# Kernel optimization log

Hardware: AMD Instinct MI355X
Metric: run time of the kernel (lower is better)

Reference implementation:

```python
import jax, jax.numpy as jnp
import numpy as np

B, T, V, E, H = 32, 40, 8000, 50, 2048


def setup_inputs() -> dict:
    key = jax.random.key(0)
    ks = jax.random.split(key, 13)
    s = 0.02  # small init scale for stability
    return {
        "features": jax.random.normal(ks[0], (B, H), dtype=jnp.float32),
        "captions": jax.random.randint(ks[1], (B, T), 0, V),
        "emb": jax.random.normal(ks[2], (V, E), dtype=jnp.float32) * s,
        "lstm_Wih": jax.random.normal(ks[3], (4 * H, E), dtype=jnp.float32) * s,
        "lstm_bih": jax.random.normal(ks[4], (4 * H,), dtype=jnp.float32) * s,
        "lstm_Whh": jax.random.normal(ks[5], (4 * H, H), dtype=jnp.float32) * s,
        "lstm_bhh": jax.random.normal(ks[6], (4 * H,), dtype=jnp.float32) * s,
        "gru_Wih": jax.random.normal(ks[7], (3 * H, H), dtype=jnp.float32) * s,
        "gru_bih": jax.random.normal(ks[8], (3 * H,), dtype=jnp.float32) * s,
        "gru_Whh": jax.random.normal(ks[9], (3 * H, H), dtype=jnp.float32) * s,
        "gru_bhh": jax.random.normal(ks[10], (3 * H,), dtype=jnp.float32) * s,
        "lin_W": jax.random.normal(ks[11], (V, H), dtype=jnp.float32) * s,
        "lin_b": jax.random.normal(ks[12], (V,), dtype=jnp.float32) * s,
    }


def reference(features, captions, emb, lstm_Wih, lstm_bih, lstm_Whh, lstm_bhh,
              gru_Wih, gru_bih, gru_Whh, gru_bhh, lin_W, lin_b):
    # Dropout layers act as identity in eval mode.
    embeddings = emb[captions]                 # [B, T, E]
    xs = jnp.swapaxes(embeddings[:, :-1], 0, 1)  # [T-1, B, E]

    def step(carry, x):
        h_l, c_l, h_g = carry
        # torch LSTMCell
        gates = x @ lstm_Wih.T + lstm_bih + h_l @ lstm_Whh.T + lstm_bhh
        i, f, g, o = jnp.split(gates, 4, axis=-1)
        c = jax.nn.sigmoid(f) * c_l + jax.nn.sigmoid(i) * jnp.tanh(g)
        h = jax.nn.sigmoid(o) * jnp.tanh(c)
        # torch GRUCell, input = lstm cell state c
        gi = c @ gru_Wih.T + gru_bih
        gh = h_g @ gru_Whh.T + gru_bhh
        r_i, z_i, n_i = jnp.split(gi, 3, axis=-1)
        r_h, z_h, n_h = jnp.split(gh, 3, axis=-1)
        r = jax.nn.sigmoid(r_i + r_h)
        z = jax.nn.sigmoid(z_i + z_h)
        n = jnp.tanh(n_i + r * n_h)
        hg = (1.0 - z) * n + z * h_g
        out = hg @ lin_W.T + lin_b              # [B, V]
        return (h, c, hg), out

    init = (features, features, features)
    _, outs = jax.lax.scan(step, init, xs)      # [T-1, B, V]
    return jnp.swapaxes(outs, 0, 1)             # [B, T-1, V]
```

## Files before the change

kernel.cpp:

```cpp
#include <hip/hip_runtime.h>

#define BB 32
#define TT 40
#define TS 39
#define VV 8000
#define EE 50
#define HH 2048

typedef short s16x8 __attribute__((ext_vector_type(8)));
typedef float f32x4 __attribute__((ext_vector_type(4)));

__device__ __forceinline__ float sigmf(float x) { return 1.0f / (1.0f + __expf(-x)); }
__device__ __forceinline__ float tanhf_fast(float x) { return 2.0f / (1.0f + __expf(-2.0f * x)) - 1.0f; }

__device__ __forceinline__ unsigned short f2bf(float x) {
    union { float f; unsigned u; } v; v.f = x;
    unsigned r = v.u + 0x7FFF + ((v.u >> 16) & 1);
    return (unsigned short)(r >> 16);
}

__global__ void convert_kernel(const float* __restrict__ src,
                               unsigned short* __restrict__ dst, int n4) {
    int i = blockIdx.x * 256 + threadIdx.x;
    if (i < n4) {
        float4 v = ((const float4*)src)[i];
        ushort4 o;
        o.x = f2bf(v.x); o.y = f2bf(v.y); o.z = f2bf(v.z); o.w = f2bf(v.w);
        ((ushort4*)dst)[i] = o;
    }
}

__global__ void embed_proj_kernel(const int* __restrict__ caps,
                                  const float* __restrict__ emb,
                                  const float* __restrict__ Wih,
                                  const float* __restrict__ bih,
                                  const float* __restrict__ bhh,
                                  float* __restrict__ xw) {
    __shared__ float elds[BB][EE];
    int t = blockIdx.y;
    int j = blockIdx.x * 256 + threadIdx.x;
    for (int idx = threadIdx.x; idx < BB * EE; idx += 256) {
        int bl = idx / EE, e = idx - bl * EE;
        elds[bl][e] = emb[(size_t)caps[bl * TT + t] * EE + e];
    }
    __syncthreads();
    float wreg[EE];
#pragma unroll
    for (int e = 0; e < EE; ++e) wreg[e] = Wih[(size_t)j * EE + e];
    float bias = bih[j] + bhh[j];
    for (int bl = 0; bl < BB; ++bl) {
        float acc = bias;
#pragma unroll
        for (int e = 0; e < EE; ++e) acc += wreg[e] * elds[bl][e];
        xw[((size_t)(t * BB + bl)) * (4 * HH) + j] = acc;
    }
}

__global__ void init_state_kernel(const float* __restrict__ feat,
                                  float* __restrict__ c32, float* __restrict__ hg32,
                                  unsigned short* __restrict__ hbf,
                                  unsigned short* __restrict__ cbf,
                                  unsigned short* __restrict__ hgbf) {
    int i = blockIdx.x * 256 + threadIdx.x;
    float v = feat[i];
    c32[i] = v; hg32[i] = v;
    unsigned short b = f2bf(v);
    hbf[i] = b; cbf[i] = b; hgbf[i] = b;
}

__global__ __launch_bounds__(1024, 4) void step1_kernel(
    const unsigned short* __restrict__ Whh,
    const unsigned short* __restrict__ gWhh,
    const float* __restrict__ gbhh,
    const float* __restrict__ xw_t,
    const unsigned short* __restrict__ hbf_in,
    const unsigned short* __restrict__ hgbf,
    float* __restrict__ c32,
    unsigned short* __restrict__ cbf,
    unsigned short* __restrict__ hbf_out,
    float* __restrict__ gh)
{
    __shared__ float lsum[4][4][32][17];
    const int tid = threadIdx.x;
    const int lane = tid & 63;
    const int w = tid >> 6;
    const int g = w >> 2;
    const int kh = w & 3;
    const int l15 = lane & 15;
    const int lq = lane >> 4;
    const int kofs = kh * 512 + lq * 8;

    const bool lstm = (blockIdx.x < 128);
    const unsigned short* Abase;
    const unsigned short* Brow;
    if (lstm) {
        int kk0 = blockIdx.x * 16;
        Brow = Whh + (size_t)(g * HH + kk0 + l15) * HH + kofs;
        Abase = hbf_in;
    } else {
        int n0 = (blockIdx.x - 128) * 64;
        Brow = gWhh + (size_t)(n0 + g * 16 + l15) * HH + kofs;
        Abase = hgbf;
    }
    const unsigned short* Arow0 = Abase + l15 * HH + kofs;
    const unsigned short* Arow1 = Arow0 + 16 * HH;

    f32x4 acc0 = {0.f, 0.f, 0.f, 0.f};
    f32x4 acc1 = {0.f, 0.f, 0.f, 0.f};
#pragma unroll 4
    for (int it = 0; it < 16; ++it) {
        s16x8 bv = *(const s16x8*)(Brow + it * 32);
        s16x8 a0 = *(const s16x8*)(Arow0 + it * 32);
        s16x8 a1 = *(const s16x8*)(Arow1 + it * 32);
        acc0 = __builtin_amdgcn_mfma_f32_16x16x32_bf16(a0, bv, acc0, 0, 0, 0);
        acc1 = __builtin_amdgcn_mfma_f32_16x16x32_bf16(a1, bv, acc1, 0, 0, 0);
    }
#pragma unroll
    for (int r = 0; r < 4; ++r) {
        lsum[g][kh][lq * 4 + r][l15]      = acc0[r];
        lsum[g][kh][16 + lq * 4 + r][l15] = acc1[r];
    }
    __syncthreads();

    if (lstm) {
        if (tid < 512) {
            int kk0 = blockIdx.x * 16;
            int kkl = tid & 15, b = tid >> 4;
            int kk = kk0 + kkl;
            const float* xwb = xw_t + (size_t)b * 4 * HH;
            float vi = lsum[0][0][b][kkl] + lsum[0][1][b][kkl] + lsum[0][2][b][kkl] + lsum[0][3][b][kkl] + xwb[kk];
            float vf = lsum[1][0][b][kkl] + lsum[1][1][b][kkl] + lsum[1][2][b][kkl] + lsum[1][3][b][kkl] + xwb[HH + kk];
            float vg = lsum[2][0][b][kkl] + lsum[2][1][b][kkl] + lsum[2][2][b][kkl] + lsum[2][3][b][kkl] + xwb[2 * HH + kk];
            float vo = lsum[3][0][b][kkl] + lsum[3][1][b][kkl] + lsum[3][2][b][kkl] + lsum[3][3][b][kkl] + xwb[3 * HH + kk];
            int idx = b * HH + kk;
            float c = sigmf(vf) * c32[idx] + sigmf(vi) * tanhf_fast(vg);
            float h = sigmf(vo) * tanhf_fast(c);
            c32[idx] = c;
            cbf[idx] = f2bf(c);
            hbf_out[idx] = f2bf(h);
        }
    } else {
        int n0 = (blockIdx.x - 128) * 64;
        for (int cell = tid; cell < 2048; cell += 1024) {
            int nl = cell & 63, b = cell >> 6;
            int s = nl >> 4, n15 = nl & 15;
            float v = lsum[s][0][b][n15] + lsum[s][1][b][n15] + lsum[s][2][b][n15] + lsum[s][3][b][n15]
                      + gbhh[n0 + nl];
            gh[b * 3 * HH + n0 + nl] = v;
        }
    }
}

__global__ __launch_bounds__(768, 3) void step2_kernel(
    const unsigned short* __restrict__ gWih,
    const float* __restrict__ gbih,
    const unsigned short* __restrict__ cbf,
    const float* __restrict__ gh,
    float* __restrict__ hg32,
    unsigned short* __restrict__ hgbf,
    unsigned short* __restrict__ hg_all_t)
{
    __shared__ float lsum[3][4][32][17];
    const int tid = threadIdx.x;
    const int lane = tid & 63;
    const int w = tid >> 6;
    const int g = w >> 2;
    const int kh = w & 3;
    const int l15 = lane & 15;
    const int lq = lane >> 4;
    const int kofs = kh * 512 + lq * 8;
    const int kk0 = blockIdx.x * 16;

    const unsigned short* Arow0 = cbf + l15 * HH + kofs;
    const unsigned short* Arow1 = Arow0 + 16 * HH;
    const unsigned short* Brow = gWih + (size_t)(g * HH + kk0 + l15) * HH + kofs;

    f32x4 acc0 = {0.f, 0.f, 0.f, 0.f};
    f32x4 acc1 = {0.f, 0.f, 0.f, 0.f};
#pragma unroll 4
    for (int it = 0; it < 16; ++it) {
        s16x8 bv = *(const s16x8*)(Brow + it * 32);
        s16x8 a0 = *(const s16x8*)(Arow0 + it * 32);
        s16x8 a1 = *(const s16x8*)(Arow1 + it * 32);
        acc0 = __builtin_amdgcn_mfma_f32_16x16x32_bf16(a0, bv, acc0, 0, 0, 0);
        acc1 = __builtin_amdgcn_mfma_f32_16x16x32_bf16(a1, bv, acc1, 0, 0, 0);
    }
#pragma unroll
    for (int r = 0; r < 4; ++r) {
        lsum[g][kh][lq * 4 + r][l15]      = acc0[r];
        lsum[g][kh][16 + lq * 4 + r][l15] = acc1[r];
    }
    __syncthreads();

    if (tid < 512) {
        int kkl = tid & 15, b = tid >> 4;
        int kk = kk0 + kkl;
        float ri = lsum[0][0][b][kkl] + lsum[0][1][b][kkl] + lsum[0][2][b][kkl] + lsum[0][3][b][kkl] + gbih[kk];
        float zi = lsum[1][0][b][kkl] + lsum[1][1][b][kkl] + lsum[1][2][b][kkl] + lsum[1][3][b][kkl] + gbih[HH + kk];
        float ni = lsum[2][0][b][kkl] + lsum[2][1][b][kkl] + lsum[2][2][b][kkl] + lsum[2][3][b][kkl] + gbih[2 * HH + kk];
        const float* ghb = gh + b * 3 * HH;
        float r = sigmf(ri + ghb[kk]);
        float z = sigmf(zi + ghb[HH + kk]);
        float n = tanhf_fast(ni + r * ghb[2 * HH + kk]);
        int idx = b * HH + kk;
        float hgn = (1.f - z) * n + z * hg32[idx];
        hg32[idx] = hgn;
        unsigned short hb = f2bf(hgn);
        hgbf[idx] = hb;
        hg_all_t[idx] = hb;
    }
}

__global__ __launch_bounds__(256) void out_gemm_kernel(
    const unsigned short* __restrict__ A,
    const unsigned short* __restrict__ Wl,
    const float* __restrict__ bl,
    float* __restrict__ out) {
    __shared__ unsigned short As[128][32];
    __shared__ unsigned short Bs[128][32];
    const int tid = threadIdx.x;
    const int lane = tid & 63;
    const int w = tid >> 6;
    const int l15 = lane & 15;
    const int lq = lane >> 4;
    const int mt = blockIdx.x, nt = blockIdx.y;
    const int mq = w >> 1, nq = w & 1;

    const int row0 = tid >> 2, kc0 = (tid & 3) * 8;
    const unsigned short* Ap0 = A + (size_t)(mt * 128 + row0) * HH + kc0;
    const unsigned short* Ap1 = A + (size_t)(mt * 128 + 64 + row0) * HH + kc0;
    const unsigned short* Bp0 = Wl + (size_t)(nt * 128 + row0) * HH + kc0;
    const unsigned short* Bp1 = Wl + (size_t)(nt * 128 + 64 + row0) * HH + kc0;

    f32x4 acc[4][4];
#pragma unroll
    for (int i = 0; i < 4; ++i)
#pragma unroll
        for (int j = 0; j < 4; ++j) acc[i][j] = (f32x4){0.f, 0.f, 0.f, 0.f};

    for (int k0 = 0; k0 < HH; k0 += 32) {
        s16x8 a0v = *(const s16x8*)(Ap0 + k0);
        s16x8 a1v = *(const s16x8*)(Ap1 + k0);
        s16x8 b0v = *(const s16x8*)(Bp0 + k0);
        s16x8 b1v = *(const s16x8*)(Bp1 + k0);
        *(s16x8*)&As[row0][kc0]      = a0v;
        *(s16x8*)&As[64 + row0][kc0] = a1v;
        *(s16x8*)&Bs[row0][kc0]      = b0v;
        *(s16x8*)&Bs[64 + row0][kc0] = b1v;
        __syncthreads();
        s16x8 af[4], bf[4];
#pragma unroll
        for (int i = 0; i < 4; ++i) af[i] = *(const s16x8*)&As[mq * 64 + i * 16 + l15][lq * 8];
#pragma unroll
        for (int j = 0; j < 4; ++j) bf[j] = *(const s16x8*)&Bs[nq * 64 + j * 16 + l15][lq * 8];
#pragma unroll
        for (int i = 0; i < 4; ++i)
#pragma unroll
            for (int j = 0; j < 4; ++j)
                acc[i][j] = __builtin_amdgcn_mfma_f32_16x16x32_bf16(af[i], bf[j], acc[i][j], 0, 0, 0);
        __syncthreads();
    }
#pragma unroll
    for (int j = 0; j < 4; ++j) {
        int n = nt * 128 + nq * 64 + j * 16 + l15;
        float bn = bl[n < VV ? n : VV - 1];
#pragma unroll
        for (int i = 0; i < 4; ++i) {
#pragma unroll
            for (int r = 0; r < 4; ++r) {
                int m = mt * 128 + mq * 64 + i * 16 + lq * 4 + r;
                if (m < TS * BB && n < VV) {
                    int t = m >> 5, b = m & 31;
                    out[((size_t)b * TS + t) * VV + n] = acc[i][j][r] + bn;
                }
            }
        }
    }
}

extern "C" void kernel_launch(void* const* d_in, const int* in_sizes, int n_in,
                              void* d_out, int out_size, void* d_ws, size_t ws_size,
                              hipStream_t stream) {
    const float* features = (const float*)d_in[0];
    const int*   captions = (const int*)d_in[1];
    const float* emb      = (const float*)d_in[2];
    const float* lstm_Wih = (const float*)d_in[3];
    const float* lstm_bih = (const float*)d_in[4];
    const float* lstm_Whh = (const float*)d_in[5];
    const float* lstm_bhh = (const float*)d_in[6];
    const float* gru_Wih  = (const float*)d_in[7];
    const float* gru_bih  = (const float*)d_in[8];
    const float* gru_Whh  = (const float*)d_in[9];
    const float* gru_bhh  = (const float*)d_in[10];
    const float* lin_W    = (const float*)d_in[11];
    const float* lin_b    = (const float*)d_in[12];
    float* out = (float*)d_out;

    unsigned short* us = (unsigned short*)d_ws;
    unsigned short* Whh_bf  = us;
    unsigned short* gWhh_bf = Whh_bf  + (size_t)8192 * HH;
    unsigned short* gWih_bf = gWhh_bf + (size_t)6144 * HH;
    unsigned short* linW_bf = gWih_bf + (size_t)6144 * HH;
    unsigned short* hbf0    = linW_bf + (size_t)VV * HH;
    unsigned short* hbf1    = hbf0 + BB * HH;
    unsigned short* cbf     = hbf1 + BB * HH;
    unsigned short* hgbf    = cbf  + BB * HH;
    unsigned short* hg_all  = hgbf + BB * HH;
    float* f32s = (float*)(hg_all + (size_t)1280 * HH);
    float* xw   = f32s;
    float* c32  = xw + (size_t)TS * BB * 4 * HH;
    float* hg32 = c32 + BB * HH;
    float* gh   = hg32 + BB * HH;

    {
        int n4;
        n4 = 8192 * HH / 4;
        convert_kernel<<<(n4 + 255) / 256, 256, 0, stream>>>(lstm_Whh, Whh_bf, n4);
        n4 = 6144 * HH / 4;
        convert_kernel<<<(n4 + 255) / 256, 256, 0, stream>>>(gru_Whh, gWhh_bf, n4);
        convert_kernel<<<(n4 + 255) / 256, 256, 0, stream>>>(gru_Wih, gWih_bf, n4);
        n4 = VV * HH / 4;
        convert_kernel<<<(n4 + 255) / 256, 256, 0, stream>>>(lin_W, linW_bf, n4);
    }

    embed_proj_kernel<<<dim3(4 * HH / 256, TS), 256, 0, stream>>>(
        captions, emb, lstm_Wih, lstm_bih, lstm_bhh, xw);

    init_state_kernel<<<(BB * HH) / 256, 256, 0, stream>>>(
        features, c32, hg32, hbf0, cbf, hgbf);

    for (int t = 0; t < TS; ++t) {
        const unsigned short* hin = (t & 1) ? hbf1 : hbf0;
        unsigned short*       hout = (t & 1) ? hbf0 : hbf1;
        step1_kernel<<<224, 1024, 0, stream>>>(
            Whh_bf, gWhh_bf, gru_bhh, xw + (size_t)t * BB * 4 * HH,
            hin, hgbf, c32, cbf, hout, gh);
        step2_kernel<<<128, 768, 0, stream>>>(
            gWih_bf, gru_bih, cbf, gh, hg32, hgbf, hg_all + (size_t)t * BB * HH);
    }

    out_gemm_kernel<<<dim3((TS * BB + 127) / 128, (VV + 127) / 128), 256, 0, stream>>>(
        hg_all, linW_bf, lin_b, out);
}
```

Measured before the change: 2.054 ms.

## Fuse per-timestep recurrent kernels into one persistent cooperative kernel with grid sync

Replaces the 78 per-step launches of step1/step2 with a single cooperative kernel of 256 blocks that loops over all timesteps and uses grid.sync between the LSTM/GRU-hidden phase and the GRU-input phase. It targets launch overhead and inter-kernel gaps on a latency-bound recurrence. In exchange, grid-wide barriers replace kernel boundaries, some blocks sit idle in each phase, and the kernel relies on all 256 blocks of 1024 threads being co-resident.

```diff
diff --git a/kernel.cpp b/kernel.cpp
--- a/kernel.cpp
+++ b/kernel.cpp
@@ -1,4 +1,7 @@
 #include <hip/hip_runtime.h>
+#include <hip/hip_cooperative_groups.h>
+
+namespace cg = cooperative_groups;
 
 #define BB 32
 #define TT 40
@@ -68,146 +71,144 @@
     hbf[i] = b; cbf[i] = b; hgbf[i] = b;
 }
 
-__global__ __launch_bounds__(1024, 4) void step1_kernel(
-    const unsigned short* __restrict__ Whh,
-    const unsigned short* __restrict__ gWhh,
-    const float* __restrict__ gbhh,
-    const float* __restrict__ xw_t,
-    const unsigned short* __restrict__ hbf_in,
-    const unsigned short* __restrict__ hgbf,
-    float* __restrict__ c32,
-    unsigned short* __restrict__ cbf,
-    unsigned short* __restrict__ hbf_out,
-    float* __restrict__ gh)
-{
+struct PKArgs {
+    const unsigned short* Whh;
+    const unsigned short* gWhh;
+    const unsigned short* gWih;
+    const float* gbhh;
+    const float* gbih;
+    const float* xw;
+    float* c32;
+    float* hg32;
+    float* gh;
+    unsigned short* hbf0;
+    unsigned short* hbf1;
+    unsigned short* cbf;
+    unsigned short* hgbf;
+    unsigned short* hg_all;
+};
+
+__global__ __launch_bounds__(1024, 4) void persistent_step_kernel(PKArgs p) {
+    cg::grid_group grid = cg::this_grid();
     __shared__ float lsum[4][4][32][17];
     const int tid = threadIdx.x;
     const int lane = tid & 63;
     const int w = tid >> 6;
+    const int l15 = lane & 15;
+    const int lq = lane >> 4;
+    const int bx = blockIdx.x;
+
     const int g = w >> 2;
     const int kh = w & 3;
-    const int l15 = lane & 15;
-    const int lq = lane >> 4;
     const int kofs = kh * 512 + lq * 8;
 
-    const bool lstm = (blockIdx.x < 128);
-    const unsigned short* Abase;
-    const unsigned short* Brow;
-    if (lstm) {
-        int kk0 = blockIdx.x * 16;
-        Brow = Whh + (size_t)(g * HH + kk0 + l15) * HH + kofs;
-        Abase = hbf_in;
-    } else {
-        int n0 = (blockIdx.x - 128) * 64;
-        Brow = gWhh + (size_t)(n0 + g * 16 + l15) * HH + kofs;
-        Abase = hgbf;
-    }
-    const unsigned short* Arow0 = Abase + l15 * HH + kofs;
-    const unsigned short* Arow1 = Arow0 + 16 * HH;
-
-    f32x4 acc0 = {0.f, 0.f, 0.f, 0.f};
-    f32x4 acc1 = {0.f, 0.f, 0.f, 0.f};
+    const unsigned short* Brow1 = nullptr;
+    if (bx < 128) {
+        Brow1 = p.Whh + (size_t)(g * HH + bx * 16 + l15) * HH + kofs;
+    } else if (bx < 224) {
+        Brow1 = p.gWhh + (size_t)((bx - 128) * 64 + g * 16 + l15) * HH + kofs;
+    }
+    const unsigned short* Brow2 = nullptr;
+    if (bx < 128 && w < 12) {
+        Brow2 = p.gWih + (size_t)(g * HH + bx * 16 + l15) * HH + kofs;
+    }
+
+    for (int t = 0; t < TS; ++t) {
+        const unsigned short* hin  = (t & 1) ? p.hbf1 : p.hbf0;
+        unsigned short*       hout = (t & 1) ? p.hbf0 : p.hbf1;
+        const float* xw_t = p.xw + (size_t)t * BB * 4 * HH;
+
+        if (bx < 224) {
+            const unsigned short* Abase = (bx < 128) ? hin : p.hgbf;
+            const unsigned short* Arow0 = Abase + l15 * HH + kofs;
+            const unsigned short* Arow1 = Arow0 + 16 * HH;
+            f32x4 acc0 = {0.f, 0.f, 0.f, 0.f};
+            f32x4 acc1 = {0.f, 0.f, 0.f, 0.f};
 #pragma unroll 4
-    for (int it = 0; it < 16; ++it) {
-        s16x8 bv = *(const s16x8*)(Brow + it * 32);
-        s16x8 a0 = *(const s16x8*)(Arow0 + it * 32);
-        s16x8 a1 = *(const s16x8*)(Arow1 + it * 32);
-        acc0 = __builtin_amdgcn_mfma_f32_16x16x32_bf16(a0, bv, acc0, 0, 0, 0);
-        acc1 = __builtin_amdgcn_mfma_f32_16x16x32_bf16(a1, bv, acc1, 0, 0, 0);
-    }
-#pragma unroll
-    for (int r = 0; r < 4; ++r) {
-        lsum[g][kh][lq * 4 + r][l15]      = acc0[r];
-        lsum[g][kh][16 + lq * 4 + r][l15] = acc1[r];
-    }
-    __syncthreads();
-
-    if (lstm) {
-        if (tid < 512) {
-            int kk0 = blockIdx.x * 16;
+            for (int it = 0; it < 16; ++it) {
+                s16x8 bv = *(const s16x8*)(Brow1 + it * 32);
+                s16x8 a0 = *(const s16x8*)(Arow0 + it * 32);
+                s16x8 a1 = *(const s16x8*)(Arow1 + it * 32);
+                acc0 = __builtin_amdgcn_mfma_f32_16x16x32_bf16(a0, bv, acc0, 0, 0, 0);
+                acc1 = __builtin_amdgcn_mfma_f32_16x16x32_bf16(a1, bv, acc1, 0, 0, 0);
+            }
+#pragma unroll
+            for (int r = 0; r < 4; ++r) {
+                lsum[g][kh][lq * 4 + r][l15]      = acc0[r];
+                lsum[g][kh][16 + lq * 4 + r][l15] = acc1[r];
+            }
+        }
+        __syncthreads();
+
+        if (bx < 128) {
+            if (tid < 512) {
+                int kk0 = bx * 16;
+                int kkl = tid & 15, b = tid >> 4;
+                int kk = kk0 + kkl;
+                const float* xwb = xw_t + (size_t)b * 4 * HH;
+                float vi = lsum[0][0][b][kkl] + lsum[0][1][b][kkl] + lsum[0][2][b][kkl] + lsum[0][3][b][kkl] + xwb[kk];
+                float vf = lsum[1][0][b][kkl] + lsum[1][1][b][kkl] + lsum[1][2][b][kkl] + lsum[1][3][b][kkl] + xwb[HH + kk];
+                float vg = lsum[2][0][b][kkl] + lsum[2][1][b][kkl] + lsum[2][2][b][kkl] + lsum[2][3][b][kkl] + xwb[2 * HH + kk];
+                float vo = lsum[3][0][b][kkl] + lsum[3][1][b][kkl] + lsum[3][2][b][kkl] + lsum[3][3][b][kkl] + xwb[3 * HH + kk];
+                int idx = b * HH + kk;
+                float c = sigmf(vf) * p.c32[idx] + sigmf(vi) * tanhf_fast(vg);
+                float h = sigmf(vo) * tanhf_fast(c);
+                p.c32[idx] = c;
+                p.cbf[idx] = f2bf(c);
+                hout[idx] = f2bf(h);
+            }
+        } else if (bx < 224) {
+            int n0 = (bx - 128) * 64;
+            for (int cell = tid; cell < 2048; cell += 1024) {
+                int nl = cell & 63, b = cell >> 6;
+                int s = nl >> 4, n15 = nl & 15;
+                float v = lsum[s][0][b][n15] + lsum[s][1][b][n15] + lsum[s][2][b][n15] + lsum[s][3][b][n15]
+                          + p.gbhh[n0 + nl];
+                p.gh[b * 3 * HH + n0 + nl] = v;
+            }
+        }
+        grid.sync();
+
+        if (bx < 128 && w < 12) {
+            const unsigned short* Arow0 = p.cbf + l15 * HH + kofs;
+            const unsigned short* Arow1 = Arow0 + 16 * HH;
+            f32x4 acc0 = {0.f, 0.f, 0.f, 0.f};
+            f32x4 acc1 = {0.f, 0.f, 0.f, 0.f};
+#pragma unroll 4
+            for (int it = 0; it < 16; ++it) {
+                s16x8 bv = *(const s16x8*)(Brow2 + it * 32);
+                s16x8 a0 = *(const s16x8*)(Arow0 + it * 32);
+                s16x8 a1 = *(const s16x8*)(Arow1 + it * 32);
+                acc0 = __builtin_amdgcn_mfma_f32_16x16x32_bf16(a0, bv, acc0, 0, 0, 0);
+                acc1 = __builtin_amdgcn_mfma_f32_16x16x32_bf16(a1, bv, acc1, 0, 0, 0);
+            }
+#pragma unroll
+            for (int r = 0; r < 4; ++r) {
+                lsum[g][kh][lq * 4 + r][l15]      = acc0[r];
+                lsum[g][kh][16 + lq * 4 + r][l15] = acc1[r];
+            }
+        }
+        __syncthreads();
+
+        if (bx < 128 && tid < 512) {
+            int kk0 = bx * 16;
             int kkl = tid & 15, b = tid >> 4;
             int kk = kk0 + kkl;
-            const float* xwb = xw_t + (size_t)b * 4 * HH;
-            float vi = lsum[0][0][b][kkl] + lsum[0][1][b][kkl] + lsum[0][2][b][kkl] + lsum[0][3][b][kkl] + xwb[kk];
-            float vf = lsum[1][0][b][kkl] + lsum[1][1][b][kkl] + lsum[1][2][b][kkl] + lsum[1][3][b][kkl] + xwb[HH + kk];
-            float vg = lsum[2][0][b][kkl] + lsum[2][1][b][kkl] + lsum[2][2][b][kkl] + lsum[2][3][b][kkl] + xwb[2 * HH + kk];
-            float vo = lsum[3][0][b][kkl] + lsum[3][1][b][kkl] + lsum[3][2][b][kkl] + lsum[3][3][b][kkl] + xwb[3 * HH + kk];
+            float ri = lsum[0][0][b][kkl] + lsum[0][1][b][kkl] + lsum[0][2][b][kkl] + lsum[0][3][b][kkl] + p.gbih[kk];
+            float zi = lsum[1][0][b][kkl] + lsum[1][1][b][kkl] + lsum[1][2][b][kkl] + lsum[1][3][b][kkl] + p.gbih[HH + kk];
+            float ni = lsum[2][0][b][kkl] + lsum[2][1][b][kkl] + lsum[2][2][b][kkl] + lsum[2][3][b][kkl] + p.gbih[2 * HH + kk];
+            const float* ghb = p.gh + b * 3 * HH;
+            float r = sigmf(ri + ghb[kk]);
+            float z = sigmf(zi + ghb[HH + kk]);
+            float n = tanhf_fast(ni + r * ghb[2 * HH + kk]);
             int idx = b * HH + kk;
-            float c = sigmf(vf) * c32[idx] + sigmf(vi) * tanhf_fast(vg);
-            float h = sigmf(vo) * tanhf_fast(c);
-            c32[idx] = c;
-            cbf[idx] = f2bf(c);
-            hbf_out[idx] = f2bf(h);
-        }
-    } else {
-        int n0 = (blockIdx.x - 128) * 64;
-        for (int cell = tid; cell < 2048; cell += 1024) {
-            int nl = cell & 63, b = cell >> 6;
-            int s = nl >> 4, n15 = nl & 15;
-            float v = lsum[s][0][b][n15] + lsum[s][1][b][n15] + lsum[s][2][b][n15] + lsum[s][3][b][n15]
-                      + gbhh[n0 + nl];
-            gh[b * 3 * HH + n0 + nl] = v;
-        }
-    }
-}
-
-__global__ __launch_bounds__(768, 3) void step2_kernel(
-    const unsigned short* __restrict__ gWih,
-    const float* __restrict__ gbih,
-    const unsigned short* __restrict__ cbf,
-    const float* __restrict__ gh,
-    float* __restrict__ hg32,
-    unsigned short* __restrict__ hgbf,
-    unsigned short* __restrict__ hg_all_t)
-{
-    __shared__ float lsum[3][4][32][17];
-    const int tid = threadIdx.x;
-    const int lane = tid & 63;
-    const int w = tid >> 6;
-    const int g = w >> 2;
-    const int kh = w & 3;
-    const int l15 = lane & 15;
-    const int lq = lane >> 4;
-    const int kofs = kh * 512 + lq * 8;
-    const int kk0 = blockIdx.x * 16;
-
-    const unsigned short* Arow0 = cbf + l15 * HH + kofs;
-    const unsigned short* Arow1 = Arow0 + 16 * HH;
-    const unsigned short* Brow = gWih + (size_t)(g * HH + kk0 + l15) * HH + kofs;
-
-    f32x4 acc0 = {0.f, 0.f, 0.f, 0.f};
-    f32x4 acc1 = {0.f, 0.f, 0.f, 0.f};
-#pragma unroll 4
-    for (int it = 0; it < 16; ++it) {
-        s16x8 bv = *(const s16x8*)(Brow + it * 32);
-        s16x8 a0 = *(const s16x8*)(Arow0 + it * 32);
-        s16x8 a1 = *(const s16x8*)(Arow1 + it * 32);
-        acc0 = __builtin_amdgcn_mfma_f32_16x16x32_bf16(a0, bv, acc0, 0, 0, 0);
-        acc1 = __builtin_amdgcn_mfma_f32_16x16x32_bf16(a1, bv, acc1, 0, 0, 0);
-    }
-#pragma unroll
-    for (int r = 0; r < 4; ++r) {
-        lsum[g][kh][lq * 4 + r][l15]      = acc0[r];
-        lsum[g][kh][16 + lq * 4 + r][l15] = acc1[r];
-    }
-    __syncthreads();
-
-    if (tid < 512) {
-        int kkl = tid & 15, b = tid >> 4;
-        int kk = kk0 + kkl;
-        float ri = lsum[0][0][b][kkl] + lsum[0][1][b][kkl] + lsum[0][2][b][kkl] + lsum[0][3][b][kkl] + gbih[kk];
-        float zi = lsum[1][0][b][kkl] + lsum[1][1][b][kkl] + lsum[1][2][b][kkl] + lsum[1][3][b][kkl] + gbih[HH + kk];
-        float ni = lsum[2][0][b][kkl] + lsum[2][1][b][kkl] + lsum[2][2][b][kkl] + lsum[2][3][b][kkl] + gbih[2 * HH + kk];
-        const float* ghb = gh + b * 3 * HH;
-        float r = sigmf(ri + ghb[kk]);
-        float z = sigmf(zi + ghb[HH + kk]);
-        float n = tanhf_fast(ni + r * ghb[2 * HH + kk]);
-        int idx = b * HH + kk;
-        float hgn = (1.f - z) * n + z * hg32[idx];
-        hg32[idx] = hgn;
-        unsigned short hb = f2bf(hgn);
-        hgbf[idx] = hb;
-        hg_all_t[idx] = hb;
+            float hgn = (1.f - z) * n + z * p.hg32[idx];
+            p.hg32[idx] = hgn;
+            unsigned short hb = f2bf(hgn);
+            p.hgbf[idx] = hb;
+            p.hg_all[(size_t)t * BB * HH + idx] = hb;
+        }
+        grid.sync();
     }
 }
 
@@ -329,14 +330,17 @@
     init_state_kernel<<<(BB * HH) / 256, 256, 0, stream>>>(
         features, c32, hg32, hbf0, cbf, hgbf);
 
-    for (int t = 0; t < TS; ++t) {
-        const unsigned short* hin = (t & 1) ? hbf1 : hbf0;
-        unsigned short*       hout = (t & 1) ? hbf0 : hbf1;
-        step1_kernel<<<224, 1024, 0, stream>>>(
-            Whh_bf, gWhh_bf, gru_bhh, xw + (size_t)t * BB * 4 * HH,
-            hin, hgbf, c32, cbf, hout, gh);
-        step2_kernel<<<128, 768, 0, stream>>>(
-            gWih_bf, gru_bih, cbf, gh, hg32, hgbf, hg_all + (size_t)t * BB * HH);
+    {
+        PKArgs pk;
+        pk.Whh = Whh_bf; pk.gWhh = gWhh_bf; pk.gWih = gWih_bf;
+        pk.gbhh = gru_bhh; pk.gbih = gru_bih;
+        pk.xw = xw;
+        pk.c32 = c32; pk.hg32 = hg32; pk.gh = gh;
+        pk.hbf0 = hbf0; pk.hbf1 = hbf1; pk.cbf = cbf; pk.hgbf = hgbf;
+        pk.hg_all = hg_all;
+        void* kargs[] = { (void*)&pk };
+        hipLaunchCooperativeKernel((const void*)persistent_step_kernel,
+                                   dim3(256), dim3(1024), kargs, 0, stream);
     }
 
     out_gemm_kernel<<<dim3((TS * BB + 127) / 128, (VV + 127) / 128), 256, 0, stream>>>(
```

Measured after the change: 4.384 ms. +113.4%, slower.
